# Optimization experiments

Hardware: AMD Instinct MI355X
Metric: run time of the kernel (lower is better)

The kernel has to match this reference:

```python
import jax, jax.numpy as jnp
import numpy as np

DIM = 4096
RATIO = 0.5
K = max(1, int(np.ceil(RATIO * DIM)))  # 2048


def setup_inputs() -> dict:
    key = jax.random.key(0)
    x = jax.random.normal(key, (4, 4096, DIM), dtype=jnp.float32)
    return {"x": x}


def reference(x):
    # Eval-mode exact path of TopKSiLU with _thr == 0:
    #   h = silu(x); thr = kth largest |h| per row; zero entries with |h| < thr.
    h = jax.nn.silu(x)
    abs_h = jnp.abs(h)
    # torch kthvalue(dim - k + 1) over ascending order == k-th largest value.
    topk_vals, _ = jax.lax.top_k(abs_h, K)          # [..., K], descending
    thr = topk_vals[..., -1:]                        # [..., 1] per-row threshold
    return jnp.where(abs_h < thr, jnp.zeros((), x.dtype), h)
```

## Files before the change

kernel.cpp:

```cpp
#include <hip/hip_runtime.h>
#include <math.h>

#define DIM      4096
#define KSEL     2048
#define NTHREADS 256
#define VPT      16
#define LO_BITS  0x3D800000u
#define HI_BITS  0x3F800000u
#define BSHIFT   17
#define CAP      256

__device__ __forceinline__ float cephes_expf_fma(float x) {
    const float LOG2EF = 1.44269504088896341f;
    const float C1     = 0.693359375f;
    const float C2     = -2.12194440e-4f;
    float z0 = __builtin_fmaf(x, LOG2EF, 0.5f);
    float fx = floorf(z0);
    float r  = __fsub_rn(x, __fmul_rn(fx, C1));
    r = __builtin_fmaf(fx, -C2, r);
    float zz = __fmul_rn(r, r);
    float y  = 1.9875691500e-4f;
    y = __builtin_fmaf(y, r, 1.3981999507e-3f);
    y = __builtin_fmaf(y, r, 8.3334519073e-3f);
    y = __builtin_fmaf(y, r, 4.1665795894e-2f);
    y = __builtin_fmaf(y, r, 1.6666665459e-1f);
    y = __builtin_fmaf(y, r, 5.0000001201e-1f);
    y = __builtin_fmaf(y, zz, r);
    y = __fadd_rn(y, 1.0f);
    int n = (int)fx;
    float scale = __int_as_float((n + 127) << 23);
    return __fmul_rn(y, scale);
}

__device__ __forceinline__ float silu_ref(float x) {
    float e = cephes_expf_fma(-x);
    float s = __fdiv_rn(1.0f, __fadd_rn(1.0f, e));
    return __fmul_rn(x, s);
}

__global__ __launch_bounds__(NTHREADS) void topk_silu_kernel(
    const float* __restrict__ x, float* __restrict__ out)
{
    const int tid  = threadIdx.x;
    const int lane = tid & 63;
    const int wave = tid >> 6;

    const float4* __restrict__ xr4 =
        reinterpret_cast<const float4*>(x + (size_t)blockIdx.x * DIM);
    float4* __restrict__ or4 =
        reinterpret_cast<float4*>(out + (size_t)blockIdx.x * DIM);

    __shared__ int      hist[256];
    __shared__ int      wred[4];
    __shared__ int      wscan[4];
    __shared__ unsigned s_dig;
    __shared__ int      s_krem;
    __shared__ int      s_nb;
    __shared__ int      s_found;
    __shared__ unsigned s_thr;
    __shared__ int      s_cnt;
    __shared__ unsigned list[CAP];

    unsigned hb[VPT];
    #pragma unroll
    for (int j = 0; j < 4; ++j) {
        float4 v = xr4[j * NTHREADS + tid];
        const float* vp = &v.x;
        #pragma unroll
        for (int c4 = 0; c4 < 4; ++c4)
            hb[j*4+c4] = __float_as_uint(silu_ref(vp[c4]));
    }

    hist[tid] = 0;
    if (tid == 0) { s_found = 0; s_cnt = 0; s_thr = 0xFFFFFFFFu; }
    __syncthreads();

    int nhi = 0;
    #pragma unroll
    for (int r = 0; r < VPT; ++r) {
        unsigned k  = hb[r] & 0x7FFFFFFFu;
        nhi += (k >= HI_BITS) ? 1 : 0;
        unsigned bk = (k - LO_BITS) >> BSHIFT;
        if (bk < 256u) atomicAdd(&hist[bk], 1);
    }
    #pragma unroll
    for (int off = 32; off; off >>= 1) nhi += __shfl_xor(nhi, off);
    if (lane == 0) wred[wave] = nhi;
    __syncthreads();
    const int n_hi = wred[0] + wred[1] + wred[2] + wred[3];

    int c = hist[tid];
    int s = c;
    #pragma unroll
    for (int off = 1; off < 64; off <<= 1) {
        int t = __shfl_down(s, off);
        if (lane + off < 64) s += t;
    }
    if (lane == 0) wscan[wave] = s;
    __syncthreads();
    #pragma unroll
    for (int w = 0; w < 4; ++w)
        if (w > wave) s += wscan[w];
    s += n_hi;

    if (s >= KSEL && s - c < KSEL) {
        s_dig   = (unsigned)tid;
        s_krem  = KSEL - (s - c);
        s_nb    = c;
        s_found = 1;
    }
    __syncthreads();

    unsigned thr_bits;
    if (s_found && s_nb <= CAP) {
        const unsigned bsel = s_dig;
        const int      krem = s_krem;
        const int      nb   = s_nb;
        #pragma unroll
        for (int r = 0; r < VPT; ++r) {
            unsigned k = hb[r] & 0x7FFFFFFFu;
            if (((k - LO_BITS) >> BSHIFT) == bsel) {
                int idx = atomicAdd(&s_cnt, 1);
                list[idx] = k;
            }
        }
        __syncthreads();
        if (tid < nb) {
            unsigned ki = list[tid];
            int rk = 0;
            for (int j = 0; j < nb; ++j) rk += (list[j] > ki) ? 1 : 0;
            if (rk < krem) atomicMin(&s_thr, ki);
        }
        __syncthreads();
        thr_bits = s_thr;
    } else {
        unsigned prefix = 0;
        int      krem   = KSEL;
        #pragma unroll 1
        for (int pass = 0; pass < 4; ++pass) {
            const int shift = 24 - pass * 8;
            hist[tid] = 0;
            __syncthreads();
            const unsigned himask =
                (pass == 0) ? 0u : (0xFFFFFFFFu << (shift + 8));
            #pragma unroll
            for (int r = 0; r < VPT; ++r) {
                unsigned k = hb[r] & 0x7FFFFFFFu;
                if ((k & himask) == prefix)
                    atomicAdd(&hist[(k >> shift) & 255u], 1);
            }
            __syncthreads();
            c = hist[tid];
            s = c;
            #pragma unroll
            for (int off = 1; off < 64; off <<= 1) {
                int t = __shfl_down(s, off);
                if (lane + off < 64) s += t;
            }
            if (lane == 0) wscan[wave] = s;
            __syncthreads();
            #pragma unroll
            for (int w = 0; w < 4; ++w)
                if (w > wave) s += wscan[w];
            if (s >= krem && s - c < krem) {
                s_dig  = (unsigned)tid;
                s_krem = krem - (s - c);
            }
            __syncthreads();
            prefix |= s_dig << shift;
            krem    = s_krem;
        }
        thr_bits = prefix;
    }

    #pragma unroll
    for (int j = 0; j < 4; ++j) {
        float4 o;
        float* op = &o.x;
        #pragma unroll
        for (int c4 = 0; c4 < 4; ++c4) {
            unsigned h = hb[j*4+c4];
            op[c4] = ((h & 0x7FFFFFFFu) >= thr_bits) ? __uint_as_float(h) : 0.0f;
        }
        or4[j * NTHREADS + tid] = o;
    }
}

extern "C" void kernel_launch(void* const* d_in, const int* in_sizes, int n_in,
                              void* d_out, int out_size, void* d_ws, size_t ws_size,
                              hipStream_t stream) {
    const float* x   = (const float*)d_in[0];
    float*       out = (float*)d_out;
    const int rows = in_sizes[0] / DIM;
    topk_silu_kernel<<<rows, NTHREADS, 0, stream>>>(x, out);
}
```

Before: 115.8 us.

## Process eight rows per block with software-prefetched next row and nontemporal stores

Each block now handles eight consecutive rows, loading the next row's inputs into registers while the current row's SiLU, histogram and threshold selection run. Histogram clearing is folded into the read step to save a barrier, output uses nontemporal stores, and launch bounds request higher occupancy. The aim is to hide global-load latency and cut per-block launch and setup cost. In exchange the grid shrinks to 2048 blocks, which may underfill the GPU, and the extra prefetch registers add pressure.

```diff
diff --git a/kernel.cpp b/kernel.cpp
--- a/kernel.cpp
+++ b/kernel.cpp
@@ -5,10 +5,13 @@
 #define KSEL     2048
 #define NTHREADS 256
 #define VPT      16
+#define RPB      8
 #define LO_BITS  0x3D800000u
 #define HI_BITS  0x3F800000u
 #define BSHIFT   17
 #define CAP      256
+
+typedef float vfloat4 __attribute__((ext_vector_type(4)));
 
 __device__ __forceinline__ float cephes_expf_fma(float x) {
     const float LOG2EF = 1.44269504088896341f;
@@ -38,17 +41,14 @@
     return __fmul_rn(x, s);
 }
 
-__global__ __launch_bounds__(NTHREADS) void topk_silu_kernel(
+__global__ __launch_bounds__(NTHREADS, 6) void topk_silu_kernel(
     const float* __restrict__ x, float* __restrict__ out)
 {
     const int tid  = threadIdx.x;
     const int lane = tid & 63;
     const int wave = tid >> 6;
 
-    const float4* __restrict__ xr4 =
-        reinterpret_cast<const float4*>(x + (size_t)blockIdx.x * DIM);
-    float4* __restrict__ or4 =
-        reinterpret_cast<float4*>(out + (size_t)blockIdx.x * DIM);
+    const size_t row0 = (size_t)blockIdx.x * RPB;
 
     __shared__ int      hist[256];
     __shared__ int      wred[4];
@@ -61,128 +61,154 @@
     __shared__ int      s_cnt;
     __shared__ unsigned list[CAP];
 
-    unsigned hb[VPT];
-    #pragma unroll
-    for (int j = 0; j < 4; ++j) {
-        float4 v = xr4[j * NTHREADS + tid];
-        const float* vp = &v.x;
-        #pragma unroll
-        for (int c4 = 0; c4 < 4; ++c4)
-            hb[j*4+c4] = __float_as_uint(silu_ref(vp[c4]));
-    }
-
     hist[tid] = 0;
     if (tid == 0) { s_found = 0; s_cnt = 0; s_thr = 0xFFFFFFFFu; }
-    __syncthreads();
-
-    int nhi = 0;
-    #pragma unroll
-    for (int r = 0; r < VPT; ++r) {
-        unsigned k  = hb[r] & 0x7FFFFFFFu;
-        nhi += (k >= HI_BITS) ? 1 : 0;
-        unsigned bk = (k - LO_BITS) >> BSHIFT;
-        if (bk < 256u) atomicAdd(&hist[bk], 1);
+
+    float4 xc[4], xn[4];
+    {
+        const float4* __restrict__ xp =
+            reinterpret_cast<const float4*>(x + row0 * DIM);
+        #pragma unroll
+        for (int j = 0; j < 4; ++j) xc[j] = xp[j * NTHREADS + tid];
     }
-    #pragma unroll
-    for (int off = 32; off; off >>= 1) nhi += __shfl_xor(nhi, off);
-    if (lane == 0) wred[wave] = nhi;
-    __syncthreads();
-    const int n_hi = wred[0] + wred[1] + wred[2] + wred[3];
-
-    int c = hist[tid];
-    int s = c;
-    #pragma unroll
-    for (int off = 1; off < 64; off <<= 1) {
-        int t = __shfl_down(s, off);
-        if (lane + off < 64) s += t;
-    }
-    if (lane == 0) wscan[wave] = s;
-    __syncthreads();
-    #pragma unroll
-    for (int w = 0; w < 4; ++w)
-        if (w > wave) s += wscan[w];
-    s += n_hi;
-
-    if (s >= KSEL && s - c < KSEL) {
-        s_dig   = (unsigned)tid;
-        s_krem  = KSEL - (s - c);
-        s_nb    = c;
-        s_found = 1;
-    }
-    __syncthreads();
-
-    unsigned thr_bits;
-    if (s_found && s_nb <= CAP) {
-        const unsigned bsel = s_dig;
-        const int      krem = s_krem;
-        const int      nb   = s_nb;
-        #pragma unroll
-        for (int r = 0; r < VPT; ++r) {
-            unsigned k = hb[r] & 0x7FFFFFFFu;
-            if (((k - LO_BITS) >> BSHIFT) == bsel) {
-                int idx = atomicAdd(&s_cnt, 1);
-                list[idx] = k;
-            }
-        }
-        __syncthreads();
-        if (tid < nb) {
-            unsigned ki = list[tid];
-            int rk = 0;
-            for (int j = 0; j < nb; ++j) rk += (list[j] > ki) ? 1 : 0;
-            if (rk < krem) atomicMin(&s_thr, ki);
-        }
-        __syncthreads();
-        thr_bits = s_thr;
-    } else {
-        unsigned prefix = 0;
-        int      krem   = KSEL;
-        #pragma unroll 1
-        for (int pass = 0; pass < 4; ++pass) {
-            const int shift = 24 - pass * 8;
-            hist[tid] = 0;
+
+    #pragma unroll 1
+    for (int r = 0; r < RPB; ++r) {
+        if (r + 1 < RPB) {
+            const float4* __restrict__ xq =
+                reinterpret_cast<const float4*>(x + (row0 + r + 1) * DIM);
+            #pragma unroll
+            for (int j = 0; j < 4; ++j) xn[j] = xq[j * NTHREADS + tid];
+        }
+
+        unsigned hb[VPT];
+        #pragma unroll
+        for (int j = 0; j < 4; ++j) {
+            const float* vp = &xc[j].x;
+            #pragma unroll
+            for (int c4 = 0; c4 < 4; ++c4)
+                hb[j*4+c4] = __float_as_uint(silu_ref(vp[c4]));
+        }
+        __syncthreads();
+
+        int nhi = 0;
+        #pragma unroll
+        for (int q = 0; q < VPT; ++q) {
+            unsigned k  = hb[q] & 0x7FFFFFFFu;
+            nhi += (k >= HI_BITS) ? 1 : 0;
+            unsigned bk = (k - LO_BITS) >> BSHIFT;
+            if (bk < 256u) atomicAdd(&hist[bk], 1);
+        }
+        #pragma unroll
+        for (int off = 32; off; off >>= 1) nhi += __shfl_xor(nhi, off);
+        if (lane == 0) wred[wave] = nhi;
+        __syncthreads();
+        const int n_hi = wred[0] + wred[1] + wred[2] + wred[3];
+
+        int c = hist[tid];
+        hist[tid] = 0;
+        int s = c;
+        #pragma unroll
+        for (int off = 1; off < 64; off <<= 1) {
+            int t = __shfl_down(s, off);
+            if (lane + off < 64) s += t;
+        }
+        if (lane == 0) wscan[wave] = s;
+        __syncthreads();
+        #pragma unroll
+        for (int w = 0; w < 4; ++w)
+            if (w > wave) s += wscan[w];
+        s += n_hi;
+
+        if (s >= KSEL && s - c < KSEL) {
+            s_dig   = (unsigned)tid;
+            s_krem  = KSEL - (s - c);
+            s_nb    = c;
+            s_found = 1;
+        }
+        __syncthreads();
+
+        unsigned thr_bits;
+        if (s_found && s_nb <= CAP) {
+            const unsigned bsel = s_dig;
+            const int      krem = s_krem;
+            const int      nb   = s_nb;
+            #pragma unroll
+            for (int q = 0; q < VPT; ++q) {
+                unsigned k = hb[q] & 0x7FFFFFFFu;
+                if (((k - LO_BITS) >> BSHIFT) == bsel) {
+                    int idx = atomicAdd(&s_cnt, 1);
+                    list[idx] = k;
+                }
+            }
             __syncthreads();
-            const unsigned himask =
-                (pass == 0) ? 0u : (0xFFFFFFFFu << (shift + 8));
-            #pragma unroll
-            for (int r = 0; r < VPT; ++r) {
-                unsigned k = hb[r] & 0x7FFFFFFFu;
-                if ((k & himask) == prefix)
-                    atomicAdd(&hist[(k >> shift) & 255u], 1);
+            if (tid < nb) {
+                unsigned ki = list[tid];
+                int rk = 0;
+                for (int j = 0; j < nb; ++j) rk += (list[j] > ki) ? 1 : 0;
+                if (rk < krem) atomicMin(&s_thr, ki);
             }
             __syncthreads();
-            c = hist[tid];
-            s = c;
-            #pragma unroll
-            for (int off = 1; off < 64; off <<= 1) {
-                int t = __shfl_down(s, off);
-                if (lane + off < 64) s += t;
-            }
-            if (lane == 0) wscan[wave] = s;
+            thr_bits = s_thr;
+        } else {
+            unsigned prefix = 0;
+            int      krem   = KSEL;
+            #pragma unroll 1
+            for (int pass = 0; pass < 4; ++pass) {
+                const int shift = 24 - pass * 8;
+                const unsigned himask =
+                    (pass == 0) ? 0u : (0xFFFFFFFFu << (shift + 8));
+                #pragma unroll
+                for (int q = 0; q < VPT; ++q) {
+                    unsigned k = hb[q] & 0x7FFFFFFFu;
+                    if ((k & himask) == prefix)
+                        atomicAdd(&hist[(k >> shift) & 255u], 1);
+                }
+                __syncthreads();
+                c = hist[tid];
+                hist[tid] = 0;
+                s = c;
+                #pragma unroll
+                for (int off = 1; off < 64; off <<= 1) {
+                    int t = __shfl_down(s, off);
+                    if (lane + off < 64) s += t;
+                }
+                if (lane == 0) wscan[wave] = s;
+                __syncthreads();
+                #pragma unroll
+                for (int w = 0; w < 4; ++w)
+                    if (w > wave) s += wscan[w];
+                if (s >= krem && s - c < krem) {
+                    s_dig  = (unsigned)tid;
+                    s_krem = krem - (s - c);
+                }
+                __syncthreads();
+                prefix |= s_dig << shift;
+                krem    = s_krem;
+            }
+            thr_bits = prefix;
+        }
+
+        vfloat4* __restrict__ oq =
+            reinterpret_cast<vfloat4*>(out + (row0 + r) * DIM);
+        #pragma unroll
+        for (int j = 0; j < 4; ++j) {
+            vfloat4 o;
+            #pragma unroll
+            for (int c4 = 0; c4 < 4; ++c4) {
+                unsigned h = hb[j*4+c4];
+                o[c4] = ((h & 0x7FFFFFFFu) >= thr_bits)
+                            ? __uint_as_float(h) : 0.0f;
+            }
+            __builtin_nontemporal_store(o, &oq[j * NTHREADS + tid]);
+        }
+
+        if (r + 1 < RPB) {
             __syncthreads();
-            #pragma unroll
-            for (int w = 0; w < 4; ++w)
-                if (w > wave) s += wscan[w];
-            if (s >= krem && s - c < krem) {
-                s_dig  = (unsigned)tid;
-                s_krem = krem - (s - c);
-            }
-            __syncthreads();
-            prefix |= s_dig << shift;
-            krem    = s_krem;
-        }
-        thr_bits = prefix;
-    }
-
-    #pragma unroll
-    for (int j = 0; j < 4; ++j) {
-        float4 o;
-        float* op = &o.x;
-        #pragma unroll
-        for (int c4 = 0; c4 < 4; ++c4) {
-            unsigned h = hb[j*4+c4];
-            op[c4] = ((h & 0x7FFFFFFFu) >= thr_bits) ? __uint_as_float(h) : 0.0f;
-        }
-        or4[j * NTHREADS + tid] = o;
+            if (tid == 0) { s_found = 0; s_cnt = 0; s_thr = 0xFFFFFFFFu; }
+            #pragma unroll
+            for (int j = 0; j < 4; ++j) xc[j] = xn[j];
+        }
     }
 }
 
@@ -192,5 +218,5 @@
     const float* x   = (const float*)d_in[0];
     float*       out = (float*)d_out;
     const int rows = in_sizes[0] / DIM;
-    topk_silu_kernel<<<rows, NTHREADS, 0, stream>>>(x, out);
-}
+    topk_silu_kernel<<<rows / RPB, NTHREADS, 0, stream>>>(x, out);
+}
```

After: 299.2 us. 2.58x slower.
